# Kernel optimization log

Measured on AMD Instinct MI355X. Metric: run time of the kernel, lower is better.

## Reference

```python
import jax, jax.numpy as jnp
import numpy as np

EPS = 1e-5  # torch LayerNorm default

def _ln(x, g, b):
    m = jnp.mean(x, axis=-1, keepdims=True)
    v = jnp.var(x, axis=-1, keepdims=True)
    return (x - m) / jnp.sqrt(v + EPS) * g + b

def setup_inputs() -> dict:
    B, S, F, H = 32, 512, 32, 128
    key = jax.random.key(0)
    ks = jax.random.split(key, 20)
    sc = 0.05
    inp = {
        "x": jax.random.normal(ks[0], (B, S, F), dtype=jnp.float32),
        # per-feature GRNs, stacked along F. fc1: Linear(1,H) -> weight vec (F,H)
        "fw1": jax.random.normal(ks[1], (F, H), dtype=jnp.float32) * sc,
        "fb1": jax.random.normal(ks[2], (F, H), dtype=jnp.float32) * sc,
        "fw2": jax.random.normal(ks[3], (F, H, H), dtype=jnp.float32) * sc,
        "fb2": jax.random.normal(ks[4], (F, H), dtype=jnp.float32) * sc,
        "fglu_w": jax.random.normal(ks[5], (F, H, 2 * H), dtype=jnp.float32) * sc,
        "fglu_b": jax.random.normal(ks[6], (F, 2 * H), dtype=jnp.float32) * sc,
        "fskip": jax.random.normal(ks[7], (F, H), dtype=jnp.float32) * sc,  # skip_proj Linear(1,H,bias=False)
        "fln_g": jnp.ones((F, H), dtype=jnp.float32),
        "fln_b": jnp.zeros((F, H), dtype=jnp.float32),
        # weight GRN: Linear(F,H)->ELU->Linear(H,F)->GLU(F)->LN(F); skip is identity (F==F)
        "ww1": jax.random.normal(ks[8], (F, H), dtype=jnp.float32) * sc,
        "wb1": jax.random.normal(ks[9], (H,), dtype=jnp.float32) * sc,
        "ww2": jax.random.normal(ks[10], (H, F), dtype=jnp.float32) * sc,
        "wb2": jax.random.normal(ks[11], (F,), dtype=jnp.float32) * sc,
        "wglu_w": jax.random.normal(ks[12], (F, 2 * F), dtype=jnp.float32) * sc,
        "wglu_b": jax.random.normal(ks[13], (2 * F,), dtype=jnp.float32) * sc,
        "wln_g": jnp.ones((F,), dtype=jnp.float32),
        "wln_b": jnp.zeros((F,), dtype=jnp.float32),
    }
    return inp

def reference(x, fw1, fb1, fw2, fb2, fglu_w, fglu_b, fskip, fln_g, fln_b,
              ww1, wb1, ww2, wb2, wglu_w, wglu_b, wln_g, wln_b):
    # ---- per-feature GRNs, batched over the F axis (dropout = eval, identity) ----
    # fc1(Linear(1,H)) + ELU : x[...,f] is a scalar per token
    h = jax.nn.elu(x[..., None] * fw1 + fb1)                 # (B,S,F,H)
    h = jnp.einsum('bsfh,fho->bsfo', h, fw2) + fb2           # fc2 (B,S,F,H)
    g = jnp.einsum('bsfh,fho->bsfo', h, fglu_w) + fglu_b     # GLU pre-act (B,S,F,2H)
    v, gate = jnp.split(g, 2, axis=-1)
    glu = v * jax.nn.sigmoid(gate)                           # (B,S,F,H)
    skip = x[..., None] * fskip                              # skip_proj (B,S,F,H)
    processed = _ln(glu + skip, fln_g[None, None], fln_b[None, None])  # (B,S,F,H)

    # ---- weight GRN over the full feature vector ----
    wh = jax.nn.elu(jnp.einsum('bsf,fh->bsh', x, ww1) + wb1)  # (B,S,H)
    wh = jnp.einsum('bsh,hf->bsf', wh, ww2) + wb2             # (B,S,F)
    wg = jnp.einsum('bsf,fg->bsg', wh, wglu_w) + wglu_b       # (B,S,2F)
    wv, wgate = jnp.split(wg, 2, axis=-1)
    wglu = wv * jax.nn.sigmoid(wgate)
    w = _ln(wglu + x, wln_g, wln_b)                           # skip is identity (F==F)
    weights = jax.nn.softmax(w, axis=-1)                      # (B,S,F)

    out = jnp.einsum('bsf,bsfh->bsh', weights, processed)     # weighted combine
    return (out, weights)
```

## Files before the change

### kernel.cpp

```cpp
#include <hip/hip_runtime.h>
#include <cstdint>
#include <cstddef>

#define NTOK 16384
#define FDIM 32
#define HDIM 128
#define TOKB 32

typedef __attribute__((ext_vector_type(8))) short short8;
typedef __attribute__((ext_vector_type(4))) float float4v;
typedef __attribute__((ext_vector_type(2))) float float2v;
typedef __attribute__((ext_vector_type(4))) unsigned int uint4v;

__device__ __forceinline__ float elu_f(float x)  { return x > 0.f ? x : __expf(x) - 1.f; }
__device__ __forceinline__ float sigm_f(float x) { return 1.f / (1.f + __expf(-x)); }

__device__ __forceinline__ unsigned int f2bf(float f) {
  unsigned int u = __float_as_uint(f);
  u += 0x7FFFu + ((u >> 16) & 1u);
  return u >> 16;
}
__device__ __forceinline__ unsigned int cvtpk(float lo, float hi) {
  unsigned int r;
  asm("v_cvt_pk_bf16_f32 %0, %1, %2" : "=v"(r) : "v"(lo), "v"(hi));
  return r;
}

__global__ __launch_bounds__(256) void k_pw(
    const float* __restrict__ x,
    const float* __restrict__ fw2, const float* __restrict__ fb2,
    const float* __restrict__ fglu_w, const float* __restrict__ fglu_b,
    const float* __restrict__ fskip, const float* __restrict__ flng,
    const float* __restrict__ flnb,
    const float* __restrict__ ww1, const float* __restrict__ wb1,
    const float* __restrict__ ww2, const float* __restrict__ wb2,
    const float* __restrict__ wglu_w, const float* __restrict__ wglu_b,
    const float* __restrict__ wln_g, const float* __restrict__ wln_b,
    unsigned short* __restrict__ bfrag, float* __restrict__ scal,
    float* __restrict__ wout)
{
  __shared__ __align__(16) float smem[4096];
  const int tid = threadIdx.x;

  if (blockIdx.x < 128) {
    const int f  = blockIdx.x >> 2;
    const int ks = blockIdx.x & 3;
    const float* src = fw2 + ((size_t)f * 128 + ks * 32) * 128;
    for (int i = 0; i < 4; ++i) {
      int vi = tid + i * 256;
      *(float4v*)&smem[vi * 4] = *(const float4v*)&src[vi * 4];
    }
    __syncthreads();

    const int o2 = tid;
    float acc[32];
#pragma unroll
    for (int kk = 0; kk < 32; ++kk) acc[kk] = 0.f;
    float bacc = 0.f;

    for (int o = 0; o < 128; o += 4) {
      float gv0 = fglu_w[((size_t)f * 128 + o + 0) * 256 + o2];
      float gv1 = fglu_w[((size_t)f * 128 + o + 1) * 256 + o2];
      float gv2 = fglu_w[((size_t)f * 128 + o + 2) * 256 + o2];
      float gv3 = fglu_w[((size_t)f * 128 + o + 3) * 256 + o2];
      bacc += fb2[f * 128 + o + 0] * gv0 + fb2[f * 128 + o + 1] * gv1
            + fb2[f * 128 + o + 2] * gv2 + fb2[f * 128 + o + 3] * gv3;
#pragma unroll
      for (int kk = 0; kk < 32; ++kk) {
        float4v a4 = *(const float4v*)&smem[kk * 128 + o];
        acc[kk] += a4[0] * gv0 + a4[1] * gv1 + a4[2] * gv2 + a4[3] * gv3;
      }
    }

    const int type = o2 >> 7;
    const int h    = o2 & 127;
    const int w2   = h >> 4;
    const int r    = h & 15;
    const size_t tbase = ((((size_t)f * 8 + w2) * 2 + type) * 4 + ks) * 512;
#pragma unroll
    for (int gg = 0; gg < 4; ++gg) {
      uint4v pk;
      pk[0] = f2bf(acc[gg * 8 + 0]) | (f2bf(acc[gg * 8 + 1]) << 16);
      pk[1] = f2bf(acc[gg * 8 + 2]) | (f2bf(acc[gg * 8 + 3]) << 16);
      pk[2] = f2bf(acc[gg * 8 + 4]) | (f2bf(acc[gg * 8 + 5]) << 16);
      pk[3] = f2bf(acc[gg * 8 + 6]) | (f2bf(acc[gg * 8 + 7]) << 16);
      *(uint4v*)(bfrag + tbase + (size_t)(r + gg * 16) * 8) = pk;
    }
    if (ks == 0) {
      scal[f * 640 + type * 128 + h] = bacc + fglu_b[f * 256 + o2];
      if (type == 0) {
        scal[f * 640 + 256 + h] = fskip[f * 128 + h];
        scal[f * 640 + 384 + h] = flng[f * 128 + h];
        scal[f * 640 + 512 + h] = flnb[f * 128 + h];
      }
    }

  } else {
    const int bid = blockIdx.x - 128;
    const int wv  = tid >> 6;
    const int l   = tid & 63;
    const int t   = bid * 4 + wv;
    float* S = smem + wv * 256;

    float xv = x[(size_t)t * 32 + (l & 31)];
    if (l < 32) S[l] = xv;
    float a0 = wb1[l], a1 = wb1[l + 64];
    __syncthreads();
    for (int f2 = 0; f2 < 32; ++f2) {
      float xf = S[f2];
      a0 = fmaf(xf, ww1[f2 * 128 + l], a0);
      a1 = fmaf(xf, ww1[f2 * 128 + l + 64], a1);
    }
    a0 = elu_f(a0); a1 = elu_f(a1);
    S[32 + l] = a0; S[32 + l + 64] = a1;
    __syncthreads();

    const int o    = l & 31;
    const int half = l >> 5;
    float b = 0.f;
    for (int hh = 0; hh < 64; ++hh)
      b = fmaf(S[32 + half * 64 + hh], ww2[(half * 64 + hh) * 32 + o], b);
    b += __shfl_xor(b, 32);
    b += wb2[o];
    S[160 + o] = b;
    __syncthreads();

    float g = wglu_b[l];
    for (int o2i = 0; o2i < 32; ++o2i)
      g = fmaf(S[160 + o2i], wglu_w[o2i * 64 + l], g);

    float gate = __shfl_xor(g, 32);
    float y = g * sigm_f(gate) + xv;
    float s = y;
    s += __shfl_xor(s, 1); s += __shfl_xor(s, 2); s += __shfl_xor(s, 4);
    s += __shfl_xor(s, 8); s += __shfl_xor(s, 16);
    float mean = s * (1.f / 32.f);
    float d = y - mean;
    float ss = d * d;
    ss += __shfl_xor(ss, 1); ss += __shfl_xor(ss, 2); ss += __shfl_xor(ss, 4);
    ss += __shfl_xor(ss, 8); ss += __shfl_xor(ss, 16);
    float rstd = rsqrtf(ss * (1.f / 32.f) + 1e-5f);
    const int cc = l & 31;
    float ln = d * rstd * wln_g[cc] + wln_b[cc];
    float mx = ln;
    mx = fmaxf(mx, __shfl_xor(mx, 1));  mx = fmaxf(mx, __shfl_xor(mx, 2));
    mx = fmaxf(mx, __shfl_xor(mx, 4));  mx = fmaxf(mx, __shfl_xor(mx, 8));
    mx = fmaxf(mx, __shfl_xor(mx, 16));
    float e = __expf(ln - mx);
    float se = e;
    se += __shfl_xor(se, 1); se += __shfl_xor(se, 2); se += __shfl_xor(se, 4);
    se += __shfl_xor(se, 8); se += __shfl_xor(se, 16);
    if (l < 32) wout[(size_t)t * 32 + l] = e / se;
  }
}

__global__ __launch_bounds__(512, 4) void k_main(
    const float* __restrict__ x,
    const float* __restrict__ fw1, const float* __restrict__ fb1,
    const unsigned short* __restrict__ bfrag, const float* __restrict__ scal,
    const float* __restrict__ wts, float* __restrict__ out)
{
  __shared__ __align__(16) unsigned short a_lds[4][TOKB * 128];
  __shared__ __align__(16) float x_lds[FDIM * TOKB];
  __shared__ __align__(16) float w_lds[FDIM * TOKB];
  __shared__ __align__(16) float sred[3][2][2][TOKB];

  const int tid = threadIdx.x;
  const int w   = tid >> 6;
  const int l   = tid & 63;
  const int tk  = l & 15;
  const int rg  = l >> 4;
  const int t0  = blockIdx.x * TOKB;
  const int h0  = w * 16 + rg * 4;
  const int st  = tid >> 4;
  const int sk  = (tid & 15) * 8;
  const int stg_byte = (st * 256 + sk * 2) ^ ((st & 7) << 4);

  {
    float2v xv = *(const float2v*)(x   + (size_t)t0 * FDIM + tid * 2);
    float2v wv = *(const float2v*)(wts + (size_t)t0 * FDIM + tid * 2);
#pragma unroll
    for (int e = 0; e < 2; ++e) {
      int flat = tid * 2 + e;
      int tt = flat >> 5, ff = flat & 31;
      x_lds[ff * TOKB + tt] = xv[e];
      w_lds[ff * TOKB + tt] = wv[e];
    }
    if (tid < 384) ((float*)sred)[tid] = 0.f;
  }

  float4v oa0 = (float4v){0.f, 0.f, 0.f, 0.f};
  float4v oa1 = (float4v){0.f, 0.f, 0.f, 0.f};
  float4v pyA0 = oa0, pyA1 = oa0, pyB0 = oa0, pyB1 = oa0;
  float4v plgA = oa0, plbA = oa0, plgB = oa0, plbB = oa0;
  float pwtA0 = 0.f, pwtA1 = 0.f, pwtB0 = 0.f, pwtB1 = 0.f;

  __syncthreads();

  int p = 0;
#pragma unroll 1
  for (int k = 0; k < FDIM / 2; ++k) {
    const int g    = 2 * k;
    const int bufp = (k & 1) * 2;

    short8 aV[4], aG[4];
    {
      const unsigned short* bb = bfrag + (((size_t)g * 8 + w) * 8) * 512 + (size_t)l * 8;
#pragma unroll
      for (int ks = 0; ks < 4; ++ks) {
        aV[ks] = *(const short8*)(bb + (size_t)ks * 512);
        aG[ks] = *(const short8*)(bb + (size_t)(4 + ks) * 512);
      }
    }

    {
      float xf = x_lds[g * TOKB + st];
      float4v w1a = *(const float4v*)(fw1 + g * HDIM + sk);
      float4v w1b = *(const float4v*)(fw1 + g * HDIM + sk + 4);
      float4v b1a = *(const float4v*)(fb1 + g * HDIM + sk);
      float4v b1b = *(const float4v*)(fb1 + g * HDIM + sk + 4);
      uint4v pk;
      pk[0] = cvtpk(elu_f(fmaf(xf, w1a[0], b1a[0])),
                    elu_f(fmaf(xf, w1a[1], b1a[1])));
      pk[1] = cvtpk(elu_f(fmaf(xf, w1a[2], b1a[2])),
                    elu_f(fmaf(xf, w1a[3], b1a[3])));
      pk[2] = cvtpk(elu_f(fmaf(xf, w1b[0], b1b[0])),
                    elu_f(fmaf(xf, w1b[1], b1b[1])));
      pk[3] = cvtpk(elu_f(fmaf(xf, w1b[2], b1b[2])),
                    elu_f(fmaf(xf, w1b[3], b1b[3])));
      *(uint4v*)((char*)a_lds[bufp] + stg_byte) = pk;
    }
    {
      float xf = x_lds[(g + 1) * TOKB + st];
      float4v w1a = *(const float4v*)(fw1 + (g + 1) * HDIM + sk);
      float4v w1b = *(const float4v*)(fw1 + (g + 1) * HDIM + sk + 4);
      float4v b1a = *(const float4v*)(fb1 + (g + 1) * HDIM + sk);
      float4v b1b = *(const float4v*)(fb1 + (g + 1) * HDIM + sk + 4);
      uint4v pk;
      pk[0] = cvtpk(elu_f(fmaf(xf, w1a[0], b1a[0])),
                    elu_f(fmaf(xf, w1a[1], b1a[1])));
      pk[1] = cvtpk(elu_f(fmaf(xf, w1a[2], b1a[2])),
                    elu_f(fmaf(xf, w1a[3], b1a[3])));
      pk[2] = cvtpk(elu_f(fmaf(xf, w1b[0], b1b[0])),
                    elu_f(fmaf(xf, w1b[1], b1b[1])));
      pk[3] = cvtpk(elu_f(fmaf(xf, w1b[2], b1b[2])),
                    elu_f(fmaf(xf, w1b[3], b1b[3])));
      *(uint4v*)((char*)a_lds[bufp + 1] + stg_byte) = pk;
    }

    __syncthreads();

    if (k > 0) {
      const int pp = (p == 0) ? 2 : p - 1;
      {
        float sA  = sred[pp][0][0][tk],      ssA = sred[pp][0][1][tk];
        float sB  = sred[pp][0][0][16 + tk], ssB = sred[pp][0][1][16 + tk];
        float m0 = sA * (1.f / 128.f);
        float m1 = sB * (1.f / 128.f);
        float v0 = fmaf(-m0, m0, ssA * (1.f / 128.f));
        float v1 = fmaf(-m1, m1, ssB * (1.f / 128.f));
        float rw0 = rsqrtf(v0 + 1e-5f) * pwtA0;
        float rw1 = rsqrtf(v1 + 1e-5f) * pwtA1;
#pragma unroll
        for (int i = 0; i < 4; ++i) {
          oa0[i] = fmaf((pyA0[i] - m0) * rw0, plgA[i], fmaf(pwtA0, plbA[i], oa0[i]));
          oa1[i] = fmaf((pyA1[i] - m1) * rw1, plgA[i], fmaf(pwtA1, plbA[i], oa1[i]));
        }
      }
      {
        float sA  = sred[pp][1][0][tk],      ssA = sred[pp][1][1][tk];
        float sB  = sred[pp][1][0][16 + tk], ssB = sred[pp][1][1][16 + tk];
        float m0 = sA * (1.f / 128.f);
        float m1 = sB * (1.f / 128.f);
        float v0 = fmaf(-m0, m0, ssA * (1.f / 128.f));
        float v1 = fmaf(-m1, m1, ssB * (1.f / 128.f));
        float rw0 = rsqrtf(v0 + 1e-5f) * pwtB0;
        float rw1 = rsqrtf(v1 + 1e-5f) * pwtB1;
#pragma unroll
        for (int i = 0; i < 4; ++i) {
          oa0[i] = fmaf((pyB0[i] - m0) * rw0, plgB[i], fmaf(pwtB0, plbB[i], oa0[i]));
          oa1[i] = fmaf((pyB1[i] - m1) * rw1, plgB[i], fmaf(pwtB1, plbB[i], oa1[i]));
        }
      }
    }

    {
      const float* sp = scal + (size_t)g * 640 + h0;
      float4v bcv = *(const float4v*)(sp);
      float4v bcg = *(const float4v*)(sp + 128);
      float4v fs4 = *(const float4v*)(sp + 256);
      float4v lg4 = *(const float4v*)(sp + 384);
      float4v lb4 = *(const float4v*)(sp + 512);

      float4v av0 = (float4v){0.f,0.f,0.f,0.f}, ag0 = av0, av1 = av0, ag1 = av0;
#pragma unroll
      for (int ks = 0; ks < 4; ++ks) {
        int b0 = tk * 256 + (ks * 32 + rg * 8) * 2;
        b0 ^= (tk & 7) << 4;
        short8 hf0 = *(const short8*)((const char*)a_lds[bufp] + b0);
        int b1 = (16 + tk) * 256 + (ks * 32 + rg * 8) * 2;
        b1 ^= (tk & 7) << 4;
        short8 hf1 = *(const short8*)((const char*)a_lds[bufp] + b1);
        av0 = __builtin_amdgcn_mfma_f32_16x16x32_bf16(aV[ks], hf0, av0, 0, 0, 0);
        ag0 = __builtin_amdgcn_mfma_f32_16x16x32_bf16(aG[ks], hf0, ag0, 0, 0, 0);
        av1 = __builtin_amdgcn_mfma_f32_16x16x32_bf16(aV[ks], hf1, av1, 0, 0, 0);
        ag1 = __builtin_amdgcn_mfma_f32_16x16x32_bf16(aG[ks], hf1, ag1, 0, 0, 0);
      }

      float xt0 = x_lds[g * TOKB + tk],      wt0 = w_lds[g * TOKB + tk];
      float xt1 = x_lds[g * TOKB + 16 + tk], wt1 = w_lds[g * TOKB + 16 + tk];
      float s0 = 0.f, ss0 = 0.f, s1 = 0.f, ss1 = 0.f;
#pragma unroll
      for (int i = 0; i < 4; ++i) {
        float ya = fmaf(xt0, fs4[i], (av0[i] + bcv[i]) * sigm_f(ag0[i] + bcg[i]));
        float yb = fmaf(xt1, fs4[i], (av1[i] + bcv[i]) * sigm_f(ag1[i] + bcg[i]));
        pyA0[i] = ya; pyA1[i] = yb;
        s0 += ya; ss0 = fmaf(ya, ya, ss0);
        s1 += yb; ss1 = fmaf(yb, yb, ss1);
      }
      s0  += __shfl_xor(s0, 16);  s0  += __shfl_xor(s0, 32);
      ss0 += __shfl_xor(ss0, 16); ss0 += __shfl_xor(ss0, 32);
      s1  += __shfl_xor(s1, 16);  s1  += __shfl_xor(s1, 32);
      ss1 += __shfl_xor(ss1, 16); ss1 += __shfl_xor(ss1, 32);
      if (rg == 0) {
        atomicAdd(&sred[p][0][0][tk], s0);
        atomicAdd(&sred[p][0][0][16 + tk], s1);
      } else if (rg == 1) {
        atomicAdd(&sred[p][0][1][tk], ss0);
        atomicAdd(&sred[p][0][1][16 + tk], ss1);
      }
      plgA = lg4; plbA = lb4; pwtA0 = wt0; pwtA1 = wt1;
    }

    {
      const unsigned short* bb = bfrag + (((size_t)(g + 1) * 8 + w) * 8) * 512 + (size_t)l * 8;
#pragma unroll
      for (int ks = 0; ks < 4; ++ks) {
        aV[ks] = *(const short8*)(bb + (size_t)ks * 512);
        aG[ks] = *(const short8*)(bb + (size_t)(4 + ks) * 512);
      }
    }

    {
      const float* sp = scal + (size_t)(g + 1) * 640 + h0;
      float4v bcv = *(const float4v*)(sp);
      float4v bcg = *(const float4v*)(sp + 128);
      float4v fs4 = *(const float4v*)(sp + 256);
      float4v lg4 = *(const float4v*)(sp + 384);
      float4v lb4 = *(const float4v*)(sp + 512);

      float4v av0 = (float4v){0.f,0.f,0.f,0.f}, ag0 = av0, av1 = av0, ag1 = av0;
#pragma unroll
      for (int ks = 0; ks < 4; ++ks) {
        int b0 = tk * 256 + (ks * 32 + rg * 8) * 2;
        b0 ^= (tk & 7) << 4;
        short8 hf0 = *(const short8*)((const char*)a_lds[bufp + 1] + b0);
        int b1 = (16 + tk) * 256 + (ks * 32 + rg * 8) * 2;
        b1 ^= (tk & 7) << 4;
        short8 hf1 = *(const short8*)((const char*)a_lds[bufp + 1] + b1);
        av0 = __builtin_amdgcn_mfma_f32_16x16x32_bf16(aV[ks], hf0, av0, 0, 0, 0);
        ag0 = __builtin_amdgcn_mfma_f32_16x16x32_bf16(aG[ks], hf0, ag0, 0, 0, 0);
        av1 = __builtin_amdgcn_mfma_f32_16x16x32_bf16(aV[ks], hf1, av1, 0, 0, 0);
        ag1 = __builtin_amdgcn_mfma_f32_16x16x32_bf16(aG[ks], hf1, ag1, 0, 0, 0);
      }

      float xt0 = x_lds[(g + 1) * TOKB + tk],      wt0 = w_lds[(g + 1) * TOKB + tk];
      float xt1 = x_lds[(g + 1) * TOKB + 16 + tk], wt1 = w_lds[(g + 1) * TOKB + 16 + tk];
      float s0 = 0.f, ss0 = 0.f, s1 = 0.f, ss1 = 0.f;
#pragma unroll
      for (int i = 0; i < 4; ++i) {
        float ya = fmaf(xt0, fs4[i], (av0[i] + bcv[i]) * sigm_f(ag0[i] + bcg[i]));
        float yb = fmaf(xt1, fs4[i], (av1[i] + bcv[i]) * sigm_f(ag1[i] + bcg[i]));
        pyB0[i] = ya; pyB1[i] = yb;
        s0 += ya; ss0 = fmaf(ya, ya, ss0);
        s1 += yb; ss1 = fmaf(yb, yb, ss1);
      }
      s0  += __shfl_xor(s0, 16);  s0  += __shfl_xor(s0, 32);
      ss0 += __shfl_xor(ss0, 16); ss0 += __shfl_xor(ss0, 32);
      s1  += __shfl_xor(s1, 16);  s1  += __shfl_xor(s1, 32);
      ss1 += __shfl_xor(ss1, 16); ss1 += __shfl_xor(ss1, 32);
      if (rg == 0) {
        atomicAdd(&sred[p][1][0][tk], s0);
        atomicAdd(&sred[p][1][0][16 + tk], s1);
      } else if (rg == 1) {
        atomicAdd(&sred[p][1][1][tk], ss0);
        atomicAdd(&sred[p][1][1][16 + tk], ss1);
      }
      plgB = lg4; plbB = lb4; pwtB0 = wt0; pwtB1 = wt1;
    }

    {
      const int pn = (p == 2) ? 0 : p + 1;
      if (tid < 128) ((float*)(sred[pn]))[tid] = 0.f;
      p = pn;
    }
  }

  __syncthreads();
  {
    const int pp = (p == 0) ? 2 : p - 1;
    {
      float sA  = sred[pp][0][0][tk],      ssA = sred[pp][0][1][tk];
      float sB  = sred[pp][0][0][16 + tk], ssB = sred[pp][0][1][16 + tk];
      float m0 = sA * (1.f / 128.f);
      float m1 = sB * (1.f / 128.f);
      float v0 = fmaf(-m0, m0, ssA * (1.f / 128.f));
      float v1 = fmaf(-m1, m1, ssB * (1.f / 128.f));
      float rw0 = rsqrtf(v0 + 1e-5f) * pwtA0;
      float rw1 = rsqrtf(v1 + 1e-5f) * pwtA1;
#pragma unroll
      for (int i = 0; i < 4; ++i) {
        oa0[i] = fmaf((pyA0[i] - m0) * rw0, plgA[i], fmaf(pwtA0, plbA[i], oa0[i]));
        oa1[i] = fmaf((pyA1[i] - m1) * rw1, plgA[i], fmaf(pwtA1, plbA[i], oa1[i]));
      }
    }
    {
      float sA  = sred[pp][1][0][tk],      ssA = sred[pp][1][1][tk];
      float sB  = sred[pp][1][0][16 + tk], ssB = sred[pp][1][1][16 + tk];
      float m0 = sA * (1.f / 128.f);
      float m1 = sB * (1.f / 128.f);
      float v0 = fmaf(-m0, m0, ssA * (1.f / 128.f));
      float v1 = fmaf(-m1, m1, ssB * (1.f / 128.f));
      float rw0 = rsqrtf(v0 + 1e-5f) * pwtB0;
      float rw1 = rsqrtf(v1 + 1e-5f) * pwtB1;
#pragma unroll
      for (int i = 0; i < 4; ++i) {
        oa0[i] = fmaf((pyB0[i] - m0) * rw0, plgB[i], fmaf(pwtB0, plbB[i], oa0[i]));
        oa1[i] = fmaf((pyB1[i] - m1) * rw1, plgB[i], fmaf(pwtB1, plbB[i], oa1[i]));
      }
    }
  }

  *(float4v*)(out + (size_t)(t0 + tk) * HDIM + h0)      = oa0;
  *(float4v*)(out + (size_t)(t0 + 16 + tk) * HDIM + h0) = oa1;
}

extern "C" void kernel_launch(void* const* d_in, const int* in_sizes, int n_in,
                              void* d_out, int out_size, void* d_ws, size_t ws_size,
                              hipStream_t stream) {
  const float* x      = (const float*)d_in[0];
  const float* fw1    = (const float*)d_in[1];
  const float* fb1    = (const float*)d_in[2];
  const float* fw2    = (const float*)d_in[3];
  const float* fb2    = (const float*)d_in[4];
  const float* fglu_w = (const float*)d_in[5];
  const float* fglu_b = (const float*)d_in[6];
  const float* fskip  = (const float*)d_in[7];
  const float* fln_g  = (const float*)d_in[8];
  const float* fln_b  = (const float*)d_in[9];
  const float* ww1    = (const float*)d_in[10];
  const float* wb1    = (const float*)d_in[11];
  const float* ww2    = (const float*)d_in[12];
  const float* wb2    = (const float*)d_in[13];
  const float* wglu_w = (const float*)d_in[14];
  const float* wglu_b = (const float*)d_in[15];
  const float* wln_g  = (const float*)d_in[16];
  const float* wln_b  = (const float*)d_in[17];

  float* outp = (float*)d_out;
  float* wout = outp + (size_t)NTOK * HDIM;

  unsigned short* bfrag = (unsigned short*)d_ws;
  float* scal = (float*)((char*)d_ws + (size_t)2 * 1024 * 1024);

  k_pw<<<dim3(128 + NTOK / 4), dim3(256), 0, stream>>>(
      x, fw2, fb2, fglu_w, fglu_b, fskip, fln_g, fln_b,
      ww1, wb1, ww2, wb2, wglu_w, wglu_b, wln_g, wln_b,
      bfrag, scal, wout);
  k_main<<<dim3(NTOK / TOKB), dim3(512), 0, stream>>>(
      x, fw1, fb1, bfrag, scal, wout, outp);
}
```

Before: 139.2 us.

## Fuse weight-GRN softmax into main kernel and split weight precompute finer

The per-token weight GRN (small MLP, GLU, LayerNorm, softmax) moves from the first kernel into the prologue of the main kernel. Each of the 8 waves computes 4 tokens and writes the weights straight to LDS and to the output. This removes the global write and read of the weights and the extra 4096 blocks in the first launch. The weight-fusion precompute kernel now uses 256 blocks, each handling 16 rows instead of 32, for more parallelism. The cost is a serial per-token prologue with several block-wide barriers, run before the main loop and reusing a_lds as scratch.

```diff
diff --git a/kernel.cpp b/kernel.cpp
--- a/kernel.cpp
+++ b/kernel.cpp
@@ -27,138 +27,79 @@
 }
 
 __global__ __launch_bounds__(256) void k_pw(
-    const float* __restrict__ x,
     const float* __restrict__ fw2, const float* __restrict__ fb2,
     const float* __restrict__ fglu_w, const float* __restrict__ fglu_b,
     const float* __restrict__ fskip, const float* __restrict__ flng,
     const float* __restrict__ flnb,
+    unsigned short* __restrict__ bfrag, float* __restrict__ scal)
+{
+  __shared__ __align__(16) float smem[2048];
+  const int tid = threadIdx.x;
+  const int f   = blockIdx.x >> 3;
+  const int ks8 = blockIdx.x & 7;
+
+  const float* src = fw2 + ((size_t)f * 128 + ks8 * 16) * 128;
+  for (int i = 0; i < 2; ++i) {
+    int vi = tid + i * 256;
+    *(float4v*)&smem[vi * 4] = *(const float4v*)&src[vi * 4];
+  }
+  __syncthreads();
+
+  const int o2 = tid;
+  float acc[16];
+#pragma unroll
+  for (int kk = 0; kk < 16; ++kk) acc[kk] = 0.f;
+  float bacc = 0.f;
+
+  for (int o = 0; o < 128; o += 4) {
+    float gv0 = fglu_w[((size_t)f * 128 + o + 0) * 256 + o2];
+    float gv1 = fglu_w[((size_t)f * 128 + o + 1) * 256 + o2];
+    float gv2 = fglu_w[((size_t)f * 128 + o + 2) * 256 + o2];
+    float gv3 = fglu_w[((size_t)f * 128 + o + 3) * 256 + o2];
+    bacc += fb2[f * 128 + o + 0] * gv0 + fb2[f * 128 + o + 1] * gv1
+          + fb2[f * 128 + o + 2] * gv2 + fb2[f * 128 + o + 3] * gv3;
+#pragma unroll
+    for (int kk = 0; kk < 16; ++kk) {
+      float4v a4 = *(const float4v*)&smem[kk * 128 + o];
+      acc[kk] += a4[0] * gv0 + a4[1] * gv1 + a4[2] * gv2 + a4[3] * gv3;
+    }
+  }
+
+  const int type = o2 >> 7;
+  const int h    = o2 & 127;
+  const int w2   = h >> 4;
+  const int r    = h & 15;
+  const int ks   = ks8 >> 1;
+  const int ggb  = (ks8 & 1) * 2;
+  const size_t tbase = ((((size_t)f * 8 + w2) * 2 + type) * 4 + ks) * 512;
+#pragma unroll
+  for (int g2 = 0; g2 < 2; ++g2) {
+    uint4v pk;
+    pk[0] = f2bf(acc[g2 * 8 + 0]) | (f2bf(acc[g2 * 8 + 1]) << 16);
+    pk[1] = f2bf(acc[g2 * 8 + 2]) | (f2bf(acc[g2 * 8 + 3]) << 16);
+    pk[2] = f2bf(acc[g2 * 8 + 4]) | (f2bf(acc[g2 * 8 + 5]) << 16);
+    pk[3] = f2bf(acc[g2 * 8 + 6]) | (f2bf(acc[g2 * 8 + 7]) << 16);
+    *(uint4v*)(bfrag + tbase + (size_t)(r + (ggb + g2) * 16) * 8) = pk;
+  }
+  if (ks8 == 0) {
+    scal[f * 640 + type * 128 + h] = bacc + fglu_b[f * 256 + o2];
+    if (type == 0) {
+      scal[f * 640 + 256 + h] = fskip[f * 128 + h];
+      scal[f * 640 + 384 + h] = flng[f * 128 + h];
+      scal[f * 640 + 512 + h] = flnb[f * 128 + h];
+    }
+  }
+}
+
+__global__ __launch_bounds__(512, 4) void k_main(
+    const float* __restrict__ x,
+    const float* __restrict__ fw1, const float* __restrict__ fb1,
+    const unsigned short* __restrict__ bfrag, const float* __restrict__ scal,
     const float* __restrict__ ww1, const float* __restrict__ wb1,
     const float* __restrict__ ww2, const float* __restrict__ wb2,
     const float* __restrict__ wglu_w, const float* __restrict__ wglu_b,
     const float* __restrict__ wln_g, const float* __restrict__ wln_b,
-    unsigned short* __restrict__ bfrag, float* __restrict__ scal,
-    float* __restrict__ wout)
-{
-  __shared__ __align__(16) float smem[4096];
-  const int tid = threadIdx.x;
-
-  if (blockIdx.x < 128) {
-    const int f  = blockIdx.x >> 2;
-    const int ks = blockIdx.x & 3;
-    const float* src = fw2 + ((size_t)f * 128 + ks * 32) * 128;
-    for (int i = 0; i < 4; ++i) {
-      int vi = tid + i * 256;
-      *(float4v*)&smem[vi * 4] = *(const float4v*)&src[vi * 4];
-    }
-    __syncthreads();
-
-    const int o2 = tid;
-    float acc[32];
-#pragma unroll
-    for (int kk = 0; kk < 32; ++kk) acc[kk] = 0.f;
-    float bacc = 0.f;
-
-    for (int o = 0; o < 128; o += 4) {
-      float gv0 = fglu_w[((size_t)f * 128 + o + 0) * 256 + o2];
-      float gv1 = fglu_w[((size_t)f * 128 + o + 1) * 256 + o2];
-      float gv2 = fglu_w[((size_t)f * 128 + o + 2) * 256 + o2];
-      float gv3 = fglu_w[((size_t)f * 128 + o + 3) * 256 + o2];
-      bacc += fb2[f * 128 + o + 0] * gv0 + fb2[f * 128 + o + 1] * gv1
-            + fb2[f * 128 + o + 2] * gv2 + fb2[f * 128 + o + 3] * gv3;
-#pragma unroll
-      for (int kk = 0; kk < 32; ++kk) {
-        float4v a4 = *(const float4v*)&smem[kk * 128 + o];
-        acc[kk] += a4[0] * gv0 + a4[1] * gv1 + a4[2] * gv2 + a4[3] * gv3;
-      }
-    }
-
-    const int type = o2 >> 7;
-    const int h    = o2 & 127;
-    const int w2   = h >> 4;
-    const int r    = h & 15;
-    const size_t tbase = ((((size_t)f * 8 + w2) * 2 + type) * 4 + ks) * 512;
-#pragma unroll
-    for (int gg = 0; gg < 4; ++gg) {
-      uint4v pk;
-      pk[0] = f2bf(acc[gg * 8 + 0]) | (f2bf(acc[gg * 8 + 1]) << 16);
-      pk[1] = f2bf(acc[gg * 8 + 2]) | (f2bf(acc[gg * 8 + 3]) << 16);
-      pk[2] = f2bf(acc[gg * 8 + 4]) | (f2bf(acc[gg * 8 + 5]) << 16);
-      pk[3] = f2bf(acc[gg * 8 + 6]) | (f2bf(acc[gg * 8 + 7]) << 16);
-      *(uint4v*)(bfrag + tbase + (size_t)(r + gg * 16) * 8) = pk;
-    }
-    if (ks == 0) {
-      scal[f * 640 + type * 128 + h] = bacc + fglu_b[f * 256 + o2];
-      if (type == 0) {
-        scal[f * 640 + 256 + h] = fskip[f * 128 + h];
-        scal[f * 640 + 384 + h] = flng[f * 128 + h];
-        scal[f * 640 + 512 + h] = flnb[f * 128 + h];
-      }
-    }
-
-  } else {
-    const int bid = blockIdx.x - 128;
-    const int wv  = tid >> 6;
-    const int l   = tid & 63;
-    const int t   = bid * 4 + wv;
-    float* S = smem + wv * 256;
-
-    float xv = x[(size_t)t * 32 + (l & 31)];
-    if (l < 32) S[l] = xv;
-    float a0 = wb1[l], a1 = wb1[l + 64];
-    __syncthreads();
-    for (int f2 = 0; f2 < 32; ++f2) {
-      float xf = S[f2];
-      a0 = fmaf(xf, ww1[f2 * 128 + l], a0);
-      a1 = fmaf(xf, ww1[f2 * 128 + l + 64], a1);
-    }
-    a0 = elu_f(a0); a1 = elu_f(a1);
-    S[32 + l] = a0; S[32 + l + 64] = a1;
-    __syncthreads();
-
-    const int o    = l & 31;
-    const int half = l >> 5;
-    float b = 0.f;
-    for (int hh = 0; hh < 64; ++hh)
-      b = fmaf(S[32 + half * 64 + hh], ww2[(half * 64 + hh) * 32 + o], b);
-    b += __shfl_xor(b, 32);
-    b += wb2[o];
-    S[160 + o] = b;
-    __syncthreads();
-
-    float g = wglu_b[l];
-    for (int o2i = 0; o2i < 32; ++o2i)
-      g = fmaf(S[160 + o2i], wglu_w[o2i * 64 + l], g);
-
-    float gate = __shfl_xor(g, 32);
-    float y = g * sigm_f(gate) + xv;
-    float s = y;
-    s += __shfl_xor(s, 1); s += __shfl_xor(s, 2); s += __shfl_xor(s, 4);
-    s += __shfl_xor(s, 8); s += __shfl_xor(s, 16);
-    float mean = s * (1.f / 32.f);
-    float d = y - mean;
-    float ss = d * d;
-    ss += __shfl_xor(ss, 1); ss += __shfl_xor(ss, 2); ss += __shfl_xor(ss, 4);
-    ss += __shfl_xor(ss, 8); ss += __shfl_xor(ss, 16);
-    float rstd = rsqrtf(ss * (1.f / 32.f) + 1e-5f);
-    const int cc = l & 31;
-    float ln = d * rstd * wln_g[cc] + wln_b[cc];
-    float mx = ln;
-    mx = fmaxf(mx, __shfl_xor(mx, 1));  mx = fmaxf(mx, __shfl_xor(mx, 2));
-    mx = fmaxf(mx, __shfl_xor(mx, 4));  mx = fmaxf(mx, __shfl_xor(mx, 8));
-    mx = fmaxf(mx, __shfl_xor(mx, 16));
-    float e = __expf(ln - mx);
-    float se = e;
-    se += __shfl_xor(se, 1); se += __shfl_xor(se, 2); se += __shfl_xor(se, 4);
-    se += __shfl_xor(se, 8); se += __shfl_xor(se, 16);
-    if (l < 32) wout[(size_t)t * 32 + l] = e / se;
-  }
-}
-
-__global__ __launch_bounds__(512, 4) void k_main(
-    const float* __restrict__ x,
-    const float* __restrict__ fw1, const float* __restrict__ fb1,
-    const unsigned short* __restrict__ bfrag, const float* __restrict__ scal,
-    const float* __restrict__ wts, float* __restrict__ out)
+    float* __restrict__ wout, float* __restrict__ out)
 {
   __shared__ __align__(16) unsigned short a_lds[4][TOKB * 128];
   __shared__ __align__(16) float x_lds[FDIM * TOKB];
@@ -177,16 +118,71 @@
   const int stg_byte = (st * 256 + sk * 2) ^ ((st & 7) << 4);
 
   {
-    float2v xv = *(const float2v*)(x   + (size_t)t0 * FDIM + tid * 2);
-    float2v wv = *(const float2v*)(wts + (size_t)t0 * FDIM + tid * 2);
+    float2v xv = *(const float2v*)(x + (size_t)t0 * FDIM + tid * 2);
 #pragma unroll
     for (int e = 0; e < 2; ++e) {
       int flat = tid * 2 + e;
       int tt = flat >> 5, ff = flat & 31;
       x_lds[ff * TOKB + tt] = xv[e];
-      w_lds[ff * TOKB + tt] = wv[e];
     }
     if (tid < 384) ((float*)sred)[tid] = 0.f;
+  }
+  __syncthreads();
+
+  {
+    float* S = ((float*)a_lds) + w * 192;
+    const int o    = l & 31;
+    const int half = l >> 5;
+#pragma unroll 1
+    for (int it = 0; it < 4; ++it) {
+      const int t = w * 4 + it;
+      float a0 = wb1[l], a1 = wb1[l + 64];
+      for (int f2 = 0; f2 < 32; ++f2) {
+        float xf = x_lds[f2 * TOKB + t];
+        a0 = fmaf(xf, ww1[f2 * 128 + l], a0);
+        a1 = fmaf(xf, ww1[f2 * 128 + l + 64], a1);
+      }
+      a0 = elu_f(a0); a1 = elu_f(a1);
+      S[l] = a0; S[64 + l] = a1;
+      __syncthreads();
+      float b = 0.f;
+      for (int hh = 0; hh < 64; ++hh)
+        b = fmaf(S[half * 64 + hh], ww2[(half * 64 + hh) * 32 + o], b);
+      b += __shfl_xor(b, 32);
+      b += wb2[o];
+      S[128 + o] = b;
+      __syncthreads();
+      float g = wglu_b[l];
+      for (int o2i = 0; o2i < 32; ++o2i)
+        g = fmaf(S[128 + o2i], wglu_w[o2i * 64 + l], g);
+      float gate = __shfl_xor(g, 32);
+      float xv2 = x_lds[(l & 31) * TOKB + t];
+      float y = g * sigm_f(gate) + xv2;
+      float s = y;
+      s += __shfl_xor(s, 1); s += __shfl_xor(s, 2); s += __shfl_xor(s, 4);
+      s += __shfl_xor(s, 8); s += __shfl_xor(s, 16);
+      float mean = s * (1.f / 32.f);
+      float d = y - mean;
+      float ss = d * d;
+      ss += __shfl_xor(ss, 1); ss += __shfl_xor(ss, 2); ss += __shfl_xor(ss, 4);
+      ss += __shfl_xor(ss, 8); ss += __shfl_xor(ss, 16);
+      float rstd = rsqrtf(ss * (1.f / 32.f) + 1e-5f);
+      float ln = d * rstd * wln_g[o] + wln_b[o];
+      float mx = ln;
+      mx = fmaxf(mx, __shfl_xor(mx, 1));  mx = fmaxf(mx, __shfl_xor(mx, 2));
+      mx = fmaxf(mx, __shfl_xor(mx, 4));  mx = fmaxf(mx, __shfl_xor(mx, 8));
+      mx = fmaxf(mx, __shfl_xor(mx, 16));
+      float e = __expf(ln - mx);
+      float se = e;
+      se += __shfl_xor(se, 1); se += __shfl_xor(se, 2); se += __shfl_xor(se, 4);
+      se += __shfl_xor(se, 8); se += __shfl_xor(se, 16);
+      float wsm = e / se;
+      if (l < 32) {
+        wout[(size_t)(t0 + t) * 32 + l] = wsm;
+        w_lds[l * TOKB + t] = wsm;
+      }
+      __syncthreads();
+    }
   }
 
   float4v oa0 = (float4v){0.f, 0.f, 0.f, 0.f};
@@ -194,8 +190,6 @@
   float4v pyA0 = oa0, pyA1 = oa0, pyB0 = oa0, pyB1 = oa0;
   float4v plgA = oa0, plbA = oa0, plgB = oa0, plbB = oa0;
   float pwtA0 = 0.f, pwtA1 = 0.f, pwtB0 = 0.f, pwtB1 = 0.f;
-
-  __syncthreads();
 
   int p = 0;
 #pragma unroll 1
@@ -463,10 +457,9 @@
   unsigned short* bfrag = (unsigned short*)d_ws;
   float* scal = (float*)((char*)d_ws + (size_t)2 * 1024 * 1024);
 
-  k_pw<<<dim3(128 + NTOK / 4), dim3(256), 0, stream>>>(
-      x, fw2, fb2, fglu_w, fglu_b, fskip, fln_g, fln_b,
-      ww1, wb1, ww2, wb2, wglu_w, wglu_b, wln_g, wln_b,
-      bfrag, scal, wout);
+  k_pw<<<dim3(256), dim3(256), 0, stream>>>(
+      fw2, fb2, fglu_w, fglu_b, fskip, fln_g, fln_b, bfrag, scal);
   k_main<<<dim3(NTOK / TOKB), dim3(512), 0, stream>>>(
-      x, fw1, fb1, bfrag, scal, wout, outp);
+      x, fw1, fb1, bfrag, scal, ww1, wb1, ww2, wb2,
+      wglu_w, wglu_b, wln_g, wln_b, wout, outp);
 }
```

Measured after the change: 195.1 us. 40.1% more time.

## Stage weight-GRN weights in LDS and process 4 tokens per wave in k_pw

Applied to the files above, without the earlier changes.

The weight-GRN branch of k_pw now runs as 256 blocks, each handling 64 tokens, instead of one block per 4 tokens. Each block loads ww1, ww2 and wglu_w into shared memory once, and every wave processes 4 tokens per iteration so each weight load feeds 4 FMAs. This cuts repeated global weight loads and block launch overhead. In exchange LDS use rises to about 54KB per block, which limits occupancy and gives fewer blocks for latency hiding.

```diff
diff --git a/kernel.cpp b/kernel.cpp
--- a/kernel.cpp
+++ b/kernel.cpp
@@ -39,7 +39,7 @@
     unsigned short* __restrict__ bfrag, float* __restrict__ scal,
     float* __restrict__ wout)
 {
-  __shared__ __align__(16) float smem[4096];
+  __shared__ __align__(16) float smem[13600];
   const int tid = threadIdx.x;
 
   if (blockIdx.x < 128) {
@@ -96,61 +96,120 @@
     }
 
   } else {
-    const int bid = blockIdx.x - 128;
-    const int wv  = tid >> 6;
-    const int l   = tid & 63;
-    const int t   = bid * 4 + wv;
-    float* S = smem + wv * 256;
-
-    float xv = x[(size_t)t * 32 + (l & 31)];
-    if (l < 32) S[l] = xv;
-    float a0 = wb1[l], a1 = wb1[l + 64];
+    float* ww1_s   = smem;
+    float* ww2_s   = smem + 4096;
+    float* wglu_s  = smem + 8192;
+    float* wb1_s   = smem + 10240;
+    float* wb2_s   = smem + 10368;
+    float* wglub_s = smem + 10400;
+    float* wlng_s  = smem + 10464;
+    float* wlnb_s  = smem + 10496;
+    const int w = tid >> 6;
+    const int l = tid & 63;
+    float* Swh  = smem + 10528 + w * 512;
+    float* Swh2 = smem + 12576 + w * 128;
+    float* Sx   = smem + 13088 + w * 128;
+
+    for (int i = 0; i < 4; ++i) {
+      int vi = tid + i * 256;
+      *(float4v*)&ww1_s[vi * 4] = *(const float4v*)&ww1[vi * 4];
+      *(float4v*)&ww2_s[vi * 4] = *(const float4v*)&ww2[vi * 4];
+    }
+    for (int i = 0; i < 2; ++i) {
+      int vi = tid + i * 256;
+      *(float4v*)&wglu_s[vi * 4] = *(const float4v*)&wglu_w[vi * 4];
+    }
+    if (tid < 128) wb1_s[tid] = wb1[tid];
+    if (tid < 64)  wglub_s[tid] = wglu_b[tid];
+    if (tid < 32) {
+      wb2_s[tid]  = wb2[tid];
+      wlng_s[tid] = wln_g[tid];
+      wlnb_s[tid] = wln_b[tid];
+    }
     __syncthreads();
-    for (int f2 = 0; f2 < 32; ++f2) {
-      float xf = S[f2];
-      a0 = fmaf(xf, ww1[f2 * 128 + l], a0);
-      a1 = fmaf(xf, ww1[f2 * 128 + l + 64], a1);
-    }
-    a0 = elu_f(a0); a1 = elu_f(a1);
-    S[32 + l] = a0; S[32 + l + 64] = a1;
-    __syncthreads();
-
+
+    const int bid2 = blockIdx.x - 128;
     const int o    = l & 31;
     const int half = l >> 5;
-    float b = 0.f;
-    for (int hh = 0; hh < 64; ++hh)
-      b = fmaf(S[32 + half * 64 + hh], ww2[(half * 64 + hh) * 32 + o], b);
-    b += __shfl_xor(b, 32);
-    b += wb2[o];
-    S[160 + o] = b;
-    __syncthreads();
-
-    float g = wglu_b[l];
-    for (int o2i = 0; o2i < 32; ++o2i)
-      g = fmaf(S[160 + o2i], wglu_w[o2i * 64 + l], g);
-
-    float gate = __shfl_xor(g, 32);
-    float y = g * sigm_f(gate) + xv;
-    float s = y;
-    s += __shfl_xor(s, 1); s += __shfl_xor(s, 2); s += __shfl_xor(s, 4);
-    s += __shfl_xor(s, 8); s += __shfl_xor(s, 16);
-    float mean = s * (1.f / 32.f);
-    float d = y - mean;
-    float ss = d * d;
-    ss += __shfl_xor(ss, 1); ss += __shfl_xor(ss, 2); ss += __shfl_xor(ss, 4);
-    ss += __shfl_xor(ss, 8); ss += __shfl_xor(ss, 16);
-    float rstd = rsqrtf(ss * (1.f / 32.f) + 1e-5f);
-    const int cc = l & 31;
-    float ln = d * rstd * wln_g[cc] + wln_b[cc];
-    float mx = ln;
-    mx = fmaxf(mx, __shfl_xor(mx, 1));  mx = fmaxf(mx, __shfl_xor(mx, 2));
-    mx = fmaxf(mx, __shfl_xor(mx, 4));  mx = fmaxf(mx, __shfl_xor(mx, 8));
-    mx = fmaxf(mx, __shfl_xor(mx, 16));
-    float e = __expf(ln - mx);
-    float se = e;
-    se += __shfl_xor(se, 1); se += __shfl_xor(se, 2); se += __shfl_xor(se, 4);
-    se += __shfl_xor(se, 8); se += __shfl_xor(se, 16);
-    if (l < 32) wout[(size_t)t * 32 + l] = e / se;
+
+#pragma unroll 1
+    for (int it = 0; it < 4; ++it) {
+      const int tb = bid2 * 64 + w * 16 + it * 4;
+
+      if (l < 32) {
+#pragma unroll
+        for (int g = 0; g < 4; ++g)
+          Sx[g * 32 + l] = x[(size_t)(tb + g) * 32 + l];
+      }
+
+      float a0[4], a1[4];
+#pragma unroll
+      for (int g = 0; g < 4; ++g) { a0[g] = wb1_s[l]; a1[g] = wb1_s[64 + l]; }
+      for (int f2 = 0; f2 < 32; ++f2) {
+        float w1a = ww1_s[f2 * 128 + l];
+        float w1b = ww1_s[f2 * 128 + 64 + l];
+#pragma unroll
+        for (int g = 0; g < 4; ++g) {
+          float xf = Sx[g * 32 + f2];
+          a0[g] = fmaf(xf, w1a, a0[g]);
+          a1[g] = fmaf(xf, w1b, a1[g]);
+        }
+      }
+#pragma unroll
+      for (int g = 0; g < 4; ++g) {
+        Swh[g * 128 + l]      = elu_f(a0[g]);
+        Swh[g * 128 + 64 + l] = elu_f(a1[g]);
+      }
+
+      float b[4] = {0.f, 0.f, 0.f, 0.f};
+      for (int hh = 0; hh < 64; ++hh) {
+        float w2v = ww2_s[(half * 64 + hh) * 32 + o];
+#pragma unroll
+        for (int g = 0; g < 4; ++g)
+          b[g] = fmaf(Swh[g * 128 + half * 64 + hh], w2v, b[g]);
+      }
+#pragma unroll
+      for (int g = 0; g < 4; ++g) {
+        b[g] += __shfl_xor(b[g], 32);
+        b[g] += wb2_s[o];
+        if (l < 32) Swh2[g * 32 + l] = b[g];
+      }
+
+      float gg4[4];
+#pragma unroll
+      for (int g = 0; g < 4; ++g) gg4[g] = wglub_s[l];
+      for (int oi = 0; oi < 32; ++oi) {
+        float wv = wglu_s[oi * 64 + l];
+#pragma unroll
+        for (int g = 0; g < 4; ++g)
+          gg4[g] = fmaf(Swh2[g * 32 + oi], wv, gg4[g]);
+      }
+
+#pragma unroll
+      for (int g = 0; g < 4; ++g) {
+        float gate = __shfl_xor(gg4[g], 32);
+        float y = gg4[g] * sigm_f(gate) + Sx[g * 32 + o];
+        float s = y;
+        s += __shfl_xor(s, 1); s += __shfl_xor(s, 2); s += __shfl_xor(s, 4);
+        s += __shfl_xor(s, 8); s += __shfl_xor(s, 16);
+        float mean = s * (1.f / 32.f);
+        float d = y - mean;
+        float ss = d * d;
+        ss += __shfl_xor(ss, 1); ss += __shfl_xor(ss, 2); ss += __shfl_xor(ss, 4);
+        ss += __shfl_xor(ss, 8); ss += __shfl_xor(ss, 16);
+        float rstd = rsqrtf(ss * (1.f / 32.f) + 1e-5f);
+        float ln = d * rstd * wlng_s[o] + wlnb_s[o];
+        float mx = ln;
+        mx = fmaxf(mx, __shfl_xor(mx, 1));  mx = fmaxf(mx, __shfl_xor(mx, 2));
+        mx = fmaxf(mx, __shfl_xor(mx, 4));  mx = fmaxf(mx, __shfl_xor(mx, 8));
+        mx = fmaxf(mx, __shfl_xor(mx, 16));
+        float e = __expf(ln - mx);
+        float se = e;
+        se += __shfl_xor(se, 1); se += __shfl_xor(se, 2); se += __shfl_xor(se, 4);
+        se += __shfl_xor(se, 8); se += __shfl_xor(se, 16);
+        if (l < 32) wout[(size_t)(tb + g) * 32 + l] = e / se;
+      }
+    }
   }
 }
 
@@ -463,7 +522,7 @@
   unsigned short* bfrag = (unsigned short*)d_ws;
   float* scal = (float*)((char*)d_ws + (size_t)2 * 1024 * 1024);
 
-  k_pw<<<dim3(128 + NTOK / 4), dim3(256), 0, stream>>>(
+  k_pw<<<dim3(384), dim3(256), 0, stream>>>(
       x, fw2, fb2, fglu_w, fglu_b, fskip, fln_g, fln_b,
       ww1, wb1, ww2, wb2, wglu_w, wglu_b, wln_g, wln_b,
       bfrag, scal, wout);
```

After: 160.6 us. 1.15x slower.
